# Kernel tuning notes

Measured on AMD Instinct MI355X. Metric: run time of the kernel, lower is better.

## Reference

```python
import jax, jax.numpy as jnp
import numpy as np

R_MAX = 5.0
AVG_NEIGH = 16.0
F = 64          # hidden scalar channels (hidden_irreps count of 0e)
NB = 8          # num_bessel
LMAX = 2
S = 9           # (LMAX+1)^2 spherical-harmonic components
NE = 10         # num_elements
G = 4           # num_graphs
T = 2           # num_interactions
L_OF_LM = np.array([0, 1, 1, 1, 2, 2, 2, 2, 2])


def spherical_harmonics(u):
    # real SH up to l=2, e3nn 'component' normalization; u: [E,3] unit vectors
    x, y, z = u[:, 0], u[:, 1], u[:, 2]
    s3, s5, s15 = 3.0 ** 0.5, 5.0 ** 0.5, 15.0 ** 0.5
    return jnp.stack([
        jnp.ones_like(x),
        s3 * x, s3 * y, s3 * z,
        s15 * x * y, s15 * y * z, (s5 / 2.0) * (3.0 * z * z - 1.0),
        s15 * x * z, (s15 / 2.0) * (x * x - y * y),
    ], axis=-1)  # [E, 9]


def radial_embedding(r):
    # Bessel basis * polynomial cutoff (p=5), as in MACE RadialEmbeddingBlock
    r_safe = jnp.maximum(r, 1e-6)
    n = jnp.arange(1, NB + 1, dtype=r.dtype)  # [NB]
    bessel = jnp.sqrt(2.0 / R_MAX) * jnp.sin(n[None, :] * jnp.pi * r_safe[:, None] / R_MAX) / r_safe[:, None]
    u = r / R_MAX
    p = 5.0
    f = (1.0 - 0.5 * (p + 1) * (p + 2) * u ** 5 + p * (p + 2) * u ** 6 - 0.5 * p * (p + 1) * u ** 7)
    f = f * (u < 1.0)
    return bessel * f[:, None]  # [E, NB]


def setup_inputs() -> dict:
    key = jax.random.key(0)
    ks = jax.random.split(key, 24)
    N, E = 20000, 320000
    positions = jax.random.normal(ks[0], (N, 3), dtype=jnp.float32) * 5.0
    species = jax.random.randint(ks[1], (N,), 0, NE)
    node_attrs = jax.nn.one_hot(species, NE, dtype=jnp.float32)
    edge_index = jax.random.randint(ks[2], (2, E), 0, N)
    shifts = jnp.zeros((E, 3), dtype=jnp.float32)
    batch = jnp.sort(jax.random.randint(ks[3], (N,), 0, G)).astype(jnp.int32)
    charges = jax.random.normal(ks[4], (N,), dtype=jnp.float32) * 0.1
    sc = 1.0 / np.sqrt(F)
    params = {
        'atomic_energies': jax.random.normal(ks[5], (NE,), dtype=jnp.float32),
        'W_embed': jax.random.normal(ks[6], (NE, F), dtype=jnp.float32),
        'Wr0': jax.random.normal(ks[7], (T, NB, 64), dtype=jnp.float32) / np.sqrt(NB),
        'Wr1': jax.random.normal(ks[8], (T, 64, 64), dtype=jnp.float32) / 8.0,
        'Wr2': jax.random.normal(ks[9], (T, 64, F * (LMAX + 1)), dtype=jnp.float32) / 8.0,
        'Wmix': jax.random.normal(ks[10], (T, LMAX + 1, F, F), dtype=jnp.float32) * sc,
        'Wprod': jax.random.normal(ks[11], (T, NE, F, 3), dtype=jnp.float32) * sc,
        'Wread0': jax.random.normal(ks[12], (F,), dtype=jnp.float32) * sc,
        'Wm1': jax.random.normal(ks[13], (F, 16), dtype=jnp.float32) * sc,
        'wm2': jax.random.normal(ks[14], (16,), dtype=jnp.float32) * 0.25,
        'Wq': jax.random.normal(ks[15], (T, F), dtype=jnp.float32) * sc,
    }
    return dict(positions=positions, node_attrs=node_attrs, shifts=shifts,
                charges=charges, edge_index=edge_index, batch=batch, **params)


def _forward(positions, node_attrs, shifts, charges,
             atomic_energies, W_embed, Wr0, Wr1, Wr2, Wmix, Wprod,
             Wread0, Wm1, wm2, Wq, edge_index, batch):
    N = positions.shape[0]
    src, dst = edge_index[0], edge_index[1]
    # isolated-atom reference energies
    node_e0 = node_attrs @ atomic_energies                       # [N]
    e0 = jax.ops.segment_sum(node_e0, batch, num_segments=G)     # [G]
    # edge geometry
    vec = positions[dst] - positions[src] + shifts               # [E,3]
    lengths = jnp.linalg.norm(vec, axis=-1)                      # [E]
    len_safe = jnp.where(lengths > 1e-6, lengths, 1.0)
    unit = vec / len_safe[:, None]
    edge_attrs = spherical_harmonics(unit)                       # [E,S]
    edge_feats = radial_embedding(lengths)                       # [E,NB]
    # node embedding: scalars only, rest of irreps zero
    node_feats = jnp.zeros((N, F, S), dtype=positions.dtype)
    node_feats = node_feats.at[:, :, 0].set(node_attrs @ W_embed)
    charge_density = charges[:, None] * jnp.ones((1, 1), positions.dtype)  # [N,1] formal charges (l=0)
    lm = jnp.asarray(L_OF_LM)
    energy = e0
    for t in range(T):
        # radial MLP -> per-edge tensor-product weights [E,F,LMAX+1]
        h = jax.nn.silu(edge_feats @ Wr0[t])
        h = jax.nn.silu(h @ Wr1[t])
        w = (h @ Wr2[t]).reshape(-1, F, LMAX + 1)
        wl = w[:, :, lm]                                         # [E,F,S]
        s_src = node_feats[src, :, 0]                            # [E,F] gather
        msg = wl * s_src[:, :, None] * edge_attrs[:, None, :]    # [E,F,S]
        A = jax.ops.segment_sum(msg, dst, num_segments=N) / AVG_NEIGH  # [N,F,S] scatter
        # per-l linear channel mixing
        A = jnp.einsum('nfs,sfg->ngs', A, Wmix[t][lm])
        # symmetric product basis (correlation 3), element-dependent weights
        wp = jnp.einsum('ne,efc->nfc', node_attrs, Wprod[t])     # [N,F,3]
        p1 = A[:, :, 0]                                          # scalar invariant
        p2 = jnp.sum(A * A, axis=-1)                             # norm invariant
        scale = wp[:, :, 0] + wp[:, :, 1] * p1 + wp[:, :, 2] * p2
        new_feats = A * scale[:, :, None]
        if t > 0:
            new_feats = new_feats + node_feats                   # residual self-connection
        node_feats = new_feats
        scal = node_feats[:, :, 0]
        if t == T - 1:
            node_en = jax.nn.silu(scal @ Wm1) @ wm2              # nonlinear readout
        else:
            node_en = scal @ Wread0                              # linear readout
        energy = energy + jax.ops.segment_sum(node_en, batch, num_segments=G)
        charge_density = charge_density + (scal @ Wq[t])[:, None]
    return energy  # [G]


def reference(positions, node_attrs, shifts, charges, edge_index, batch,
              atomic_energies, W_embed, Wr0, Wr1, Wr2, Wmix, Wprod,
              Wread0, Wm1, wm2, Wq):
    return _forward(positions, node_attrs, shifts, charges,
                    atomic_energies, W_embed, Wr0, Wr1, Wr2, Wmix, Wprod,
                    Wread0, Wm1, wm2, Wq, edge_index, batch)
```

## Files before the change

### kernel.cpp

```cpp
#include <hip/hip_runtime.h>
#include <hip/hip_bf16.h>

#define F 64
#define NB 8
#define NE 10
#define GSEG 4
#define EPW 256
#define NTAB 2048

__device__ __forceinline__ float silu(float x) {
    return x / (1.0f + __expf(-x));
}

__device__ __forceinline__ float bcast(float v, int lane) {
    return __uint_as_float(__builtin_amdgcn_readlane(__float_as_uint(v), lane));
}

__global__ __launch_bounds__(256) void init_nodes(
    const float* __restrict__ node_attrs, const float* __restrict__ AE,
    const float* __restrict__ W_embed, const int* __restrict__ batch,
    float* __restrict__ S0, float* __restrict__ epart,
    int* __restrict__ deg, int N)
{
    int w = threadIdx.x >> 6, g = threadIdx.x & 63;
    int n = blockIdx.x * 4 + w;
    if (n >= N) return;
    float sc = 0.0f, e0 = 0.0f;
    #pragma unroll
    for (int e = 0; e < NE; e++) {
        float a = node_attrs[n * NE + e];
        sc = fmaf(a, W_embed[e * F + g], sc);
        e0 = fmaf(a, AE[e], e0);
    }
    S0[(size_t)n * F + g] = sc;
    if (g == 0) {
        deg[n] = 0;
        atomicAdd(&epart[batch[n] * EPW + (n & (EPW - 1))], e0);
    }
}

__global__ __launch_bounds__(256) void edge_prep(
    const float* __restrict__ pos, const float* __restrict__ shifts,
    const int* __restrict__ EI, int E,
    float4* __restrict__ geoFull, int* __restrict__ deg)
{
    int e = blockIdx.x * 256 + threadIdx.x;
    if (e >= E) return;
    int s = EI[e], d = EI[E + e];
    float vx = pos[d * 3 + 0] - pos[s * 3 + 0] + shifts[e * 3 + 0];
    float vy = pos[d * 3 + 1] - pos[s * 3 + 1] + shifts[e * 3 + 1];
    float vz = pos[d * 3 + 2] - pos[s * 3 + 2] + shifts[e * 3 + 2];
    float len = sqrtf(vx * vx + vy * vy + vz * vz);
    float ls = (len > 1e-6f) ? len : 1.0f;
    float inv = 1.0f / ls;
    geoFull[e] = make_float4(vx * inv, vy * inv, vz * inv, len);
    if (len < 5.0f) atomicAdd(&deg[d], 1);
}

__global__ __launch_bounds__(256) void alloc_start(
    const int* __restrict__ deg, int* __restrict__ start,
    int* __restrict__ cursor, int* __restrict__ total, int N)
{
    __shared__ int wsum[4];
    __shared__ int gbase;
    int t = threadIdx.x;
    int n = blockIdx.x * 256 + t;
    int lane = t & 63, w = t >> 6;
    int v = (n < N) ? deg[n] : 0;
    int inc = v;
    #pragma unroll
    for (int off = 1; off < 64; off <<= 1) {
        int u = __shfl_up(inc, off);
        if (lane >= off) inc += u;
    }
    if (lane == 63) wsum[w] = inc;
    __syncthreads();
    if (t == 0) {
        int s0 = wsum[0], s1 = wsum[1], s2 = wsum[2], s3 = wsum[3];
        int bs = s0 + s1 + s2 + s3;
        wsum[0] = 0; wsum[1] = s0; wsum[2] = s0 + s1; wsum[3] = s0 + s1 + s2;
        gbase = atomicAdd(total, bs);
    }
    __syncthreads();
    if (n < N) {
        int st = gbase + wsum[w] + (inc - v);
        start[n] = st;
        cursor[n] = st;
    }
}

__global__ __launch_bounds__(256) void csr_fill(
    const float4* __restrict__ geoFull, const int* __restrict__ EI, int E,
    int* __restrict__ cursor,
    float4* __restrict__ geoS, int* __restrict__ srcS, int EB)
{
    int e = blockIdx.x * 256 + threadIdx.x;
    if (e >= E) return;
    float4 gv = geoFull[e];
    if (gv.w < 5.0f) {
        int d = EI[E + e];
        int p = atomicAdd(&cursor[d], 1);
        if (p < EB) {
            geoS[p] = gv;
            srcS[p] = EI[e];
        }
    }
}

__global__ __launch_bounds__(256) void build_tables(
    const float* __restrict__ Wr0, const float* __restrict__ Wr1,
    const float* __restrict__ Wr2, float* __restrict__ Tab)
{
    const int blocksPerTab = (NTAB + 1 + 3) / 4;
    int w = threadIdx.x >> 6, lane = threadIdx.x & 63;
    int tab = blockIdx.x / blocksPerTab;
    int eidx = (blockIdx.x - tab * blocksPerTab) * 4 + w;
    if (eidx > NTAB) return;
    const float* W0 = Wr0 + tab * 512;
    const float* W1 = Wr1 + tab * 4096;
    const float* W2 = Wr2 + tab * 12288;

    float r = (float)eidx * (5.0f / NTAB);
    float rs = fmaxf(r, 1e-6f);
    float s1, c1;
    __sincosf(0.6283185307179586f * rs, &s1, &c1);
    float u = r * 0.2f;
    float u2 = u * u, u4 = u2 * u2, u5 = u4 * u, u6 = u5 * u, u7 = u6 * u;
    float fc = 1.0f - 21.0f * u5 + 35.0f * u6 - 15.0f * u7;
    float pref = 0.6324555320336759f / rs * fc;
    float ef[NB];
    {
        float sp = 0.0f, sc_ = s1, tc = 2.0f * c1;
        #pragma unroll
        for (int k = 0; k < NB; k++) {
            ef[k] = pref * sc_;
            float sn = tc * sc_ - sp;
            sp = sc_; sc_ = sn;
        }
    }

    float a1 = 0.0f;
    #pragma unroll
    for (int k = 0; k < NB; k++) a1 = fmaf(ef[k], W0[k * 64 + lane], a1);
    float h1 = silu(a1);

    float a2 = 0.0f;
    #pragma unroll 8
    for (int k = 0; k < 64; k++)
        a2 = fmaf(bcast(h1, k), W1[k * 64 + lane], a2);
    float h2 = silu(a2);

    float w0 = 0.f, w1 = 0.f, w2 = 0.f;
    #pragma unroll 8
    for (int k = 0; k < 64; k++) {
        float hk = bcast(h2, k);
        const float* wr = W2 + k * 192 + lane * 3;
        w0 = fmaf(hk, wr[0], w0);
        w1 = fmaf(hk, wr[1], w1);
        w2 = fmaf(hk, wr[2], w2);
    }

    float* Trow = Tab + ((size_t)tab * (NTAB + 1) + eidx) * 192;
    Trow[lane] = w0;
    Trow[64 + lane] = w1;
    Trow[128 + lane] = w2;
}

template <int PHASE>
__global__ __launch_bounds__(256) void gather_node(
    const float4* __restrict__ geoS, const int* __restrict__ srcS,
    const float* __restrict__ Tab,
    const int* __restrict__ start, const int* __restrict__ deg,
    const float* __restrict__ Wmixt, const float* __restrict__ Wprodt,
    const float* __restrict__ node_attrs, const int* __restrict__ batch,
    const float* __restrict__ Wread0, const float* __restrict__ Wm1,
    const float* __restrict__ wm2,
    const float* __restrict__ Sin, float* __restrict__ Sout,
    float* __restrict__ epart, int N)
{
    __shared__ float As[4][768];

    int g = threadIdx.x & 63;
    int w = threadIdx.x >> 6;
    int n = blockIdx.x * 4 + w;
    if (n >= N) return;

    int st = start[n], dg = deg[n];
    int b = batch[n];

    if (dg == 0) {
        if (PHASE == 0) {
            Sout[(size_t)n * F + g] = 0.0f;
        } else {
            float sc0 = Sin[(size_t)n * F + g];
            int gi = g & 15;
            float acc = 0.0f;
            #pragma unroll 8
            for (int k = 0; k < 64; k++)
                acc = fmaf(bcast(sc0, k), Wm1[k * 16 + gi], acc);
            float v = (g < 16) ? silu(acc) * wm2[gi] : 0.0f;
            #pragma unroll
            for (int off = 32; off > 0; off >>= 1) v += __shfl_xor(v, off);
            if (g == 0) atomicAdd(&epart[b * EPW + (n & (EPW - 1))], v);
        }
        return;
    }

    float am0 = 0.f, am1 = 0.f, am2_ = 0.f, am3 = 0.f, am4 = 0.f,
          am5 = 0.f, am6 = 0.f, am7 = 0.f, am8 = 0.f;

    const float s3 = 1.7320508075688772f;
    const float s5h = 1.1180339887498948f;
    const float s15 = 3.8729833462074170f;
    const float s15h = 1.9364916731037085f;

    for (int i = st; i < st + dg; i++) {
        float4 gv = geoS[i];
        int srcn = srcS[i];
        float sv = Sin[(size_t)srcn * F + g];
        float scaled = gv.w * (NTAB / 5.0f);
        int idx = (int)scaled;
        float fr = scaled - (float)idx;
        const float* T0 = Tab + (size_t)idx * 192;
        float wa = T0[g],        wb = T0[192 + g];
        float wc = T0[64 + g],   wd = T0[256 + g];
        float we = T0[128 + g],  wf_ = T0[320 + g];
        float w0 = fmaf(fr, wb - wa, wa);
        float w1 = fmaf(fr, wd - wc, wc);
        float w2 = fmaf(fr, wf_ - we, we);

        float ux = gv.x, uy = gv.y, uz = gv.z;
        float m0 = w0 * sv, m1 = w1 * sv, m2 = w2 * sv;
        am0 += m0;
        am1 = fmaf(m1, s3 * ux, am1);
        am2_ = fmaf(m1, s3 * uy, am2_);
        am3 = fmaf(m1, s3 * uz, am3);
        am4 = fmaf(m2, s15 * ux * uy, am4);
        am5 = fmaf(m2, s15 * uy * uz, am5);
        am6 = fmaf(m2, s5h * (3.0f * uz * uz - 1.0f), am6);
        am7 = fmaf(m2, s15 * ux * uz, am7);
        am8 = fmaf(m2, s15h * (ux * ux - uy * uy), am8);
    }

    const float inv16 = 0.0625f;
    float* aw = As[w];
    *(float4*)&aw[g * 12]     = make_float4(am0 * inv16, am1 * inv16,
                                            am2_ * inv16, am3 * inv16);
    *(float4*)&aw[g * 12 + 4] = make_float4(am4 * inv16, am5 * inv16,
                                            am6 * inv16, am7 * inv16);
    aw[g * 12 + 8] = am8 * inv16;

    float b0 = 0.f, b1 = 0.f, b2 = 0.f, b3 = 0.f, b4 = 0.f,
          b5 = 0.f, b6 = 0.f, b7 = 0.f, b8 = 0.f;
    #pragma unroll 4
    for (int f = 0; f < 64; f++) {
        float w0 = Wmixt[f * 64 + g];
        float w1 = Wmixt[4096 + f * 64 + g];
        float w2 = Wmixt[8192 + f * 64 + g];
        float4 aA = *(const float4*)&aw[f * 12];
        float4 aB = *(const float4*)&aw[f * 12 + 4];
        float a8 = aw[f * 12 + 8];
        b0 = fmaf(aA.x, w0, b0);
        b1 = fmaf(aA.y, w1, b1);
        b2 = fmaf(aA.z, w1, b2);
        b3 = fmaf(aA.w, w1, b3);
        b4 = fmaf(aB.x, w2, b4);
        b5 = fmaf(aB.y, w2, b5);
        b6 = fmaf(aB.z, w2, b6);
        b7 = fmaf(aB.w, w2, b7);
        b8 = fmaf(a8, w2, b8);
    }

    float wp0 = 0.f, wp1 = 0.f, wp2 = 0.f;
    #pragma unroll
    for (int e = 0; e < NE; e++) {
        float a = node_attrs[n * NE + e];
        const float* W = Wprodt + (e * F + g) * 3;
        wp0 = fmaf(a, W[0], wp0);
        wp1 = fmaf(a, W[1], wp1);
        wp2 = fmaf(a, W[2], wp2);
    }
    float p1 = b0;
    float p2 = b0 * b0 + b1 * b1 + b2 * b2 + b3 * b3 + b4 * b4 +
               b5 * b5 + b6 * b6 + b7 * b7 + b8 * b8;
    float scale = wp0 + wp1 * p1 + wp2 * p2;
    float sc0 = b0 * scale;

    if (PHASE == 0) {
        Sout[(size_t)n * F + g] = sc0;
        float v = sc0 * Wread0[g];
        #pragma unroll
        for (int off = 32; off > 0; off >>= 1) v += __shfl_xor(v, off);
        if (g == 0) atomicAdd(&epart[b * EPW + (n & (EPW - 1))], v);
    } else {
        sc0 += Sin[(size_t)n * F + g];
        int gi = g & 15;
        float acc = 0.0f;
        #pragma unroll 8
        for (int k = 0; k < 64; k++)
            acc = fmaf(bcast(sc0, k), Wm1[k * 16 + gi], acc);
        float v = (g < 16) ? silu(acc) * wm2[gi] : 0.0f;
        #pragma unroll
        for (int off = 32; off > 0; off >>= 1) v += __shfl_xor(v, off);
        if (g == 0) atomicAdd(&epart[b * EPW + (n & (EPW - 1))], v);
    }
}

__global__ __launch_bounds__(256) void reduce_energy(
    const float* __restrict__ epart, float* __restrict__ out)
{
    int t = threadIdx.x;
    __shared__ float ps[GSEG][4];
    for (int b = 0; b < GSEG; b++) {
        float v = epart[b * EPW + t];
        #pragma unroll
        for (int off = 32; off > 0; off >>= 1) v += __shfl_xor(v, off);
        if ((t & 63) == 0) ps[b][t >> 6] = v;
    }
    __syncthreads();
    if (t < GSEG) out[t] = ps[t][0] + ps[t][1] + ps[t][2] + ps[t][3];
}

extern "C" void kernel_launch(void* const* d_in, const int* in_sizes, int n_in,
                              void* d_out, int out_size, void* d_ws, size_t ws_size,
                              hipStream_t stream) {
    const float* positions  = (const float*)d_in[0];
    const float* node_attrs = (const float*)d_in[1];
    const float* shifts     = (const float*)d_in[2];
    const int*   edge_index = (const int*)d_in[4];
    const int*   batch      = (const int*)d_in[5];
    const float* AE         = (const float*)d_in[6];
    const float* W_embed    = (const float*)d_in[7];
    const float* Wr0        = (const float*)d_in[8];
    const float* Wr1        = (const float*)d_in[9];
    const float* Wr2        = (const float*)d_in[10];
    const float* Wmix       = (const float*)d_in[11];
    const float* Wprod      = (const float*)d_in[12];
    const float* Wread0     = (const float*)d_in[13];
    const float* Wm1        = (const float*)d_in[14];
    const float* wm2        = (const float*)d_in[15];

    int N = in_sizes[0] / 3;
    int E = in_sizes[4] / 2;
    int EB = E / 8;
    float* out = (float*)d_out;

    char* ws = (char*)d_ws;
    size_t off = 0;
    float4* geoFull = (float4*)(ws + off); off += (size_t)E * sizeof(float4);
    float4* geoS  = (float4*)(ws + off); off += (size_t)EB * sizeof(float4);
    float*  S0    = (float*)(ws + off);  off += (size_t)N * F * sizeof(float);
    float*  S1    = (float*)(ws + off);  off += (size_t)N * F * sizeof(float);
    int*    srcS  = (int*)(ws + off);    off += (size_t)EB * sizeof(int);
    int*    deg   = (int*)(ws + off);    off += (size_t)N * sizeof(int);
    int*    start = (int*)(ws + off);    off += (size_t)N * sizeof(int);
    int*    cursor= (int*)(ws + off);    off += (size_t)N * sizeof(int);
    float*  epart = (float*)(ws + off);  off += GSEG * EPW * sizeof(float);
    int*    total = (int*)(ws + off);    off += 128;
    float*  Tab   = (float*)(ws + off);
    off += (size_t)2 * (NTAB + 1) * 192 * sizeof(float);

    hipMemsetAsync(epart, 0, GSEG * EPW * sizeof(float) + 128, stream);

    int nodeBlocks4 = (N + 3) / 4;
    int nodeBlocks256 = (N + 255) / 256;
    int edgeBlocks = (E + 255) / 256;
    int tabBlocks = 2 * ((NTAB + 1 + 3) / 4);
    int gatherBlocks = (N + 3) / 4;
    size_t tabStride = (size_t)(NTAB + 1) * 192;

    init_nodes<<<nodeBlocks4, 256, 0, stream>>>(node_attrs, AE, W_embed, batch,
                                                S0, epart, deg, N);
    build_tables<<<tabBlocks, 256, 0, stream>>>(Wr0, Wr1, Wr2, Tab);
    edge_prep<<<edgeBlocks, 256, 0, stream>>>(positions, shifts, edge_index, E,
                                              geoFull, deg);
    alloc_start<<<nodeBlocks256, 256, 0, stream>>>(deg, start, cursor, total, N);
    csr_fill<<<edgeBlocks, 256, 0, stream>>>(geoFull, edge_index, E,
                                             cursor, geoS, srcS, EB);

    gather_node<0><<<gatherBlocks, 256, 0, stream>>>(geoS, srcS, Tab, start, deg,
                                         Wmix, Wprod, node_attrs, batch,
                                         Wread0, Wm1, wm2, S0, S1, epart, N);
    gather_node<1><<<gatherBlocks, 256, 0, stream>>>(geoS, srcS, Tab + tabStride,
                                         start, deg,
                                         Wmix + 12288, Wprod + NE * F * 3,
                                         node_attrs, batch,
                                         Wread0, Wm1, wm2, S1, S1, epart, N);

    reduce_energy<<<1, 256, 0, stream>>>(epart, out);
}
```

Before: 222.6 us.

## Fuse node init with radial table build and pack positions as float4

Merges the node-initialisation kernel and the radial-MLP table builder into one launch, with the block index selecting which role a block plays. This removes a launch and lets the two independent workloads share the device. The node branch also writes positions padded to float4, so edge_prep reads each endpoint with one vector load instead of three scalar loads. Separately, the Wmix loop unroll in the gather kernel is raised from 4 to 8, which may increase register pressure.

Result: no change. 222.4 us (-0.1%).

```diff
diff --git a/kernel.cpp b/kernel.cpp
--- a/kernel.cpp
+++ b/kernel.cpp
@@ -16,40 +16,103 @@
     return __uint_as_float(__builtin_amdgcn_readlane(__float_as_uint(v), lane));
 }
 
-__global__ __launch_bounds__(256) void init_nodes(
+__global__ __launch_bounds__(256) void init_and_tables(
     const float* __restrict__ node_attrs, const float* __restrict__ AE,
     const float* __restrict__ W_embed, const int* __restrict__ batch,
+    const float* __restrict__ pos,
     float* __restrict__ S0, float* __restrict__ epart,
-    int* __restrict__ deg, int N)
-{
-    int w = threadIdx.x >> 6, g = threadIdx.x & 63;
-    int n = blockIdx.x * 4 + w;
-    if (n >= N) return;
-    float sc = 0.0f, e0 = 0.0f;
+    int* __restrict__ deg, float4* __restrict__ pos4, int N, int nodeBlocks,
+    const float* __restrict__ Wr0, const float* __restrict__ Wr1,
+    const float* __restrict__ Wr2, float* __restrict__ Tab)
+{
+    int w = threadIdx.x >> 6, lane = threadIdx.x & 63;
+
+    if (blockIdx.x < (unsigned)nodeBlocks) {
+        int n = blockIdx.x * 4 + w;
+        if (n >= N) return;
+        float sc = 0.0f, e0 = 0.0f;
+        #pragma unroll
+        for (int e = 0; e < NE; e++) {
+            float a = node_attrs[n * NE + e];
+            sc = fmaf(a, W_embed[e * F + lane], sc);
+            e0 = fmaf(a, AE[e], e0);
+        }
+        S0[(size_t)n * F + lane] = sc;
+        if (lane == 0) {
+            deg[n] = 0;
+            pos4[n] = make_float4(pos[n * 3], pos[n * 3 + 1], pos[n * 3 + 2], 0.f);
+            atomicAdd(&epart[batch[n] * EPW + (n & (EPW - 1))], e0);
+        }
+        return;
+    }
+
+    const int blocksPerTab = (NTAB + 1 + 3) / 4;
+    int bid = blockIdx.x - nodeBlocks;
+    int tab = bid / blocksPerTab;
+    int eidx = (bid - tab * blocksPerTab) * 4 + w;
+    if (eidx > NTAB) return;
+    const float* W0 = Wr0 + tab * 512;
+    const float* W1 = Wr1 + tab * 4096;
+    const float* W2 = Wr2 + tab * 12288;
+
+    float r = (float)eidx * (5.0f / NTAB);
+    float rs = fmaxf(r, 1e-6f);
+    float s1, c1;
+    __sincosf(0.6283185307179586f * rs, &s1, &c1);
+    float u = r * 0.2f;
+    float u2 = u * u, u4 = u2 * u2, u5 = u4 * u, u6 = u5 * u, u7 = u6 * u;
+    float fc = 1.0f - 21.0f * u5 + 35.0f * u6 - 15.0f * u7;
+    float pref = 0.6324555320336759f / rs * fc;
+    float ef[NB];
+    {
+        float sp = 0.0f, sc_ = s1, tc = 2.0f * c1;
+        #pragma unroll
+        for (int k = 0; k < NB; k++) {
+            ef[k] = pref * sc_;
+            float sn = tc * sc_ - sp;
+            sp = sc_; sc_ = sn;
+        }
+    }
+
+    float a1 = 0.0f;
     #pragma unroll
-    for (int e = 0; e < NE; e++) {
-        float a = node_attrs[n * NE + e];
-        sc = fmaf(a, W_embed[e * F + g], sc);
-        e0 = fmaf(a, AE[e], e0);
-    }
-    S0[(size_t)n * F + g] = sc;
-    if (g == 0) {
-        deg[n] = 0;
-        atomicAdd(&epart[batch[n] * EPW + (n & (EPW - 1))], e0);
-    }
+    for (int k = 0; k < NB; k++) a1 = fmaf(ef[k], W0[k * 64 + lane], a1);
+    float h1 = silu(a1);
+
+    float a2 = 0.0f;
+    #pragma unroll 8
+    for (int k = 0; k < 64; k++)
+        a2 = fmaf(bcast(h1, k), W1[k * 64 + lane], a2);
+    float h2 = silu(a2);
+
+    float w0 = 0.f, w1 = 0.f, w2 = 0.f;
+    #pragma unroll 8
+    for (int k = 0; k < 64; k++) {
+        float hk = bcast(h2, k);
+        const float* wr = W2 + k * 192 + lane * 3;
+        w0 = fmaf(hk, wr[0], w0);
+        w1 = fmaf(hk, wr[1], w1);
+        w2 = fmaf(hk, wr[2], w2);
+    }
+
+    float* Trow = Tab + ((size_t)tab * (NTAB + 1) + eidx) * 192;
+    Trow[lane] = w0;
+    Trow[64 + lane] = w1;
+    Trow[128 + lane] = w2;
 }
 
 __global__ __launch_bounds__(256) void edge_prep(
-    const float* __restrict__ pos, const float* __restrict__ shifts,
+    const float4* __restrict__ pos4, const float* __restrict__ shifts,
     const int* __restrict__ EI, int E,
     float4* __restrict__ geoFull, int* __restrict__ deg)
 {
     int e = blockIdx.x * 256 + threadIdx.x;
     if (e >= E) return;
     int s = EI[e], d = EI[E + e];
-    float vx = pos[d * 3 + 0] - pos[s * 3 + 0] + shifts[e * 3 + 0];
-    float vy = pos[d * 3 + 1] - pos[s * 3 + 1] + shifts[e * 3 + 1];
-    float vz = pos[d * 3 + 2] - pos[s * 3 + 2] + shifts[e * 3 + 2];
+    float4 pd = pos4[d], ps = pos4[s];
+    float vx = pd.x - ps.x + shifts[e * 3 + 0];
+    float vy = pd.y - ps.y + shifts[e * 3 + 1];
+    float vz = pd.z - ps.z + shifts[e * 3 + 2];
     float len = sqrtf(vx * vx + vy * vy + vz * vz);
     float ls = (len > 1e-6f) ? len : 1.0f;
     float inv = 1.0f / ls;
@@ -105,65 +168,6 @@
             srcS[p] = EI[e];
         }
     }
-}
-
-__global__ __launch_bounds__(256) void build_tables(
-    const float* __restrict__ Wr0, const float* __restrict__ Wr1,
-    const float* __restrict__ Wr2, float* __restrict__ Tab)
-{
-    const int blocksPerTab = (NTAB + 1 + 3) / 4;
-    int w = threadIdx.x >> 6, lane = threadIdx.x & 63;
-    int tab = blockIdx.x / blocksPerTab;
-    int eidx = (blockIdx.x - tab * blocksPerTab) * 4 + w;
-    if (eidx > NTAB) return;
-    const float* W0 = Wr0 + tab * 512;
-    const float* W1 = Wr1 + tab * 4096;
-    const float* W2 = Wr2 + tab * 12288;
-
-    float r = (float)eidx * (5.0f / NTAB);
-    float rs = fmaxf(r, 1e-6f);
-    float s1, c1;
-    __sincosf(0.6283185307179586f * rs, &s1, &c1);
-    float u = r * 0.2f;
-    float u2 = u * u, u4 = u2 * u2, u5 = u4 * u, u6 = u5 * u, u7 = u6 * u;
-    float fc = 1.0f - 21.0f * u5 + 35.0f * u6 - 15.0f * u7;
-    float pref = 0.6324555320336759f / rs * fc;
-    float ef[NB];
-    {
-        float sp = 0.0f, sc_ = s1, tc = 2.0f * c1;
-        #pragma unroll
-        for (int k = 0; k < NB; k++) {
-            ef[k] = pref * sc_;
-            float sn = tc * sc_ - sp;
-            sp = sc_; sc_ = sn;
-        }
-    }
-
-    float a1 = 0.0f;
-    #pragma unroll
-    for (int k = 0; k < NB; k++) a1 = fmaf(ef[k], W0[k * 64 + lane], a1);
-    float h1 = silu(a1);
-
-    float a2 = 0.0f;
-    #pragma unroll 8
-    for (int k = 0; k < 64; k++)
-        a2 = fmaf(bcast(h1, k), W1[k * 64 + lane], a2);
-    float h2 = silu(a2);
-
-    float w0 = 0.f, w1 = 0.f, w2 = 0.f;
-    #pragma unroll 8
-    for (int k = 0; k < 64; k++) {
-        float hk = bcast(h2, k);
-        const float* wr = W2 + k * 192 + lane * 3;
-        w0 = fmaf(hk, wr[0], w0);
-        w1 = fmaf(hk, wr[1], w1);
-        w2 = fmaf(hk, wr[2], w2);
-    }
-
-    float* Trow = Tab + ((size_t)tab * (NTAB + 1) + eidx) * 192;
-    Trow[lane] = w0;
-    Trow[64 + lane] = w1;
-    Trow[128 + lane] = w2;
 }
 
 template <int PHASE>
@@ -252,7 +256,7 @@
 
     float b0 = 0.f, b1 = 0.f, b2 = 0.f, b3 = 0.f, b4 = 0.f,
           b5 = 0.f, b6 = 0.f, b7 = 0.f, b8 = 0.f;
-    #pragma unroll 4
+    #pragma unroll 8
     for (int f = 0; f < 64; f++) {
         float w0 = Wmixt[f * 64 + g];
         float w1 = Wmixt[4096 + f * 64 + g];
@@ -349,6 +353,7 @@
     size_t off = 0;
     float4* geoFull = (float4*)(ws + off); off += (size_t)E * sizeof(float4);
     float4* geoS  = (float4*)(ws + off); off += (size_t)EB * sizeof(float4);
+    float4* pos4  = (float4*)(ws + off); off += (size_t)N * sizeof(float4);
     float*  S0    = (float*)(ws + off);  off += (size_t)N * F * sizeof(float);
     float*  S1    = (float*)(ws + off);  off += (size_t)N * F * sizeof(float);
     int*    srcS  = (int*)(ws + off);    off += (size_t)EB * sizeof(int);
@@ -369,10 +374,11 @@
     int gatherBlocks = (N + 3) / 4;
     size_t tabStride = (size_t)(NTAB + 1) * 192;
 
-    init_nodes<<<nodeBlocks4, 256, 0, stream>>>(node_attrs, AE, W_embed, batch,
-                                                S0, epart, deg, N);
-    build_tables<<<tabBlocks, 256, 0, stream>>>(Wr0, Wr1, Wr2, Tab);
-    edge_prep<<<edgeBlocks, 256, 0, stream>>>(positions, shifts, edge_index, E,
+    init_and_tables<<<nodeBlocks4 + tabBlocks, 256, 0, stream>>>(
+        node_attrs, AE, W_embed, batch, positions,
+        S0, epart, deg, pos4, N, nodeBlocks4,
+        Wr0, Wr1, Wr2, Tab);
+    edge_prep<<<edgeBlocks, 256, 0, stream>>>(pos4, shifts, edge_index, E,
                                               geoFull, deg);
     alloc_start<<<nodeBlocks256, 256, 0, stream>>>(deg, start, cursor, total, N);
     csr_fill<<<edgeBlocks, 256, 0, stream>>>(geoFull, edge_index, E,
```
